# Kernel tuning notes

Hardware: AMD Instinct MI355X
Metric: run time of the kernel (lower is better)

The kernel has to match this reference:

```python
import jax, jax.numpy as jnp
import numpy as np

K_SIZE = 3
CH_IN = 256
NFILT = 256

def setup_inputs() -> dict:
    key = jax.random.key(0)
    k1, k2 = jax.random.split(key)
    x = jax.random.normal(k1, (32, 56, 56, CH_IN), dtype=jnp.float32)
    stdv = 1.0 / np.sqrt(K_SIZE * K_SIZE * CH_IN)
    w = jax.random.normal(k2, (K_SIZE, K_SIZE, CH_IN, NFILT), dtype=jnp.float32) * stdv
    pruning_mask = jnp.ones((K_SIZE * K_SIZE * CH_IN, NFILT), dtype=jnp.float32)
    return {"x": x, "w": w, "pruning_mask": pruning_mask}

def _magnitude_aware_weight(w):
    # scale = mean |w| over (kh, kw, cin), per output filter; stop-gradient
    scale = jax.lax.stop_gradient(jnp.mean(jnp.abs(w), axis=(0, 1, 2), keepdims=True))
    bw_no_grad = scale * jnp.sign(w)
    clipped = jnp.clip(w, -1.0, 1.0)
    # STE: forward = scale*sign(w), backward = d(clip(w,-1,1))
    return jax.lax.stop_gradient(bw_no_grad) - jax.lax.stop_gradient(clipped) + clipped

def reference(x, w, pruning_mask):
    kernel = _magnitude_aware_weight(w) * pruning_mask.reshape(K_SIZE, K_SIZE, CH_IN, NFILT)
    out = jax.lax.conv_general_dilated(
        x, kernel,
        window_strides=(1, 1),
        padding="SAME",
        dimension_numbers=("NHWC", "HWIO", "NHWC"),
    )
    return out
```

## Files before the change

kernel.cpp:

```cpp
#include <hip/hip_runtime.h>

typedef unsigned short u16;
typedef u16 u16x8 __attribute__((ext_vector_type(8)));
typedef __bf16 bf16x8 __attribute__((ext_vector_type(8)));
typedef float f32x4 __attribute__((ext_vector_type(4)));

#define NPIX 100352
#define KTOT 2304
#define IMG_PAD (58 * 58 * 256)

static __device__ __forceinline__ u16 f2bf(float f) {
  unsigned u = __float_as_uint(f);
  return (u16)((u + 0x7fffu + ((u >> 16) & 1u)) >> 16);
}

static __device__ __forceinline__ void gld_lds16(const u16* g, u16* l) {
  __builtin_amdgcn_global_load_lds(
      (const __attribute__((address_space(1))) void*)g,
      (__attribute__((address_space(3))) void*)l, 16, 0, 0);
}

__global__ void scale_accum_k(const float* __restrict__ w, float* __restrict__ scale) {
  const int t = threadIdx.x;
  const float* p = w + (long)blockIdx.x * 64 * 256 + t;
  float acc = 0.f;
#pragma unroll
  for (int e = 0; e < 64; ++e) acc += fabsf(p[(long)e * 256]);
  atomicAdd(&scale[t], acc);
}

__global__ void pack_w_k(const float* __restrict__ w, const float* __restrict__ mask,
                         const float* __restrict__ ssum, u16* __restrict__ wp) {
  __shared__ u16 t[128][33];
  const int k0 = blockIdx.x * 32;
  const int f0 = blockIdx.y * 128;
  const int tid = threadIdx.x;
#pragma unroll
  for (int i = 0; i < 16; ++i) {
    int idx = tid + i * 256;
    int kk = idx >> 7;
    int ff = idx & 127;
    long g = (long)(k0 + kk) * 256 + f0 + ff;
    float wv = w[g];
    float mv = mask[g];
    float sc = ssum[f0 + ff] * (1.0f / 2304.0f);
    float sg = (wv > 0.f) ? 1.f : ((wv < 0.f) ? -1.f : 0.f);
    t[ff][kk] = f2bf(sc * sg * mv);
  }
  __syncthreads();
#pragma unroll
  for (int i = 0; i < 8; ++i) {
    int idx = tid + i * 256;
    int row = idx >> 4;
    int c = idx & 15;
    unsigned v = (unsigned)t[row][2 * c] | ((unsigned)t[row][2 * c + 1] << 16);
    *(unsigned*)(wp + (long)(f0 + row) * KTOT + k0 + 2 * c) = v;
  }
}

__global__ __launch_bounds__(256) void fill_xpad3_k(const float* __restrict__ x,
                                                    u16* __restrict__ xp) {
  const int img = blockIdx.y;
  const int ph = blockIdx.x;
  u16* rowp = xp + ((img * 58 + ph) * 58) * 256;
  const bool irow = (ph >= 1 && ph <= 56);
  const float* xrow = x + ((long)img * 3136 + (ph - 1) * 56) * 256;
  for (int i = threadIdx.x; i < 58 * 32; i += 256) {
    const int pw = i >> 5;
    const int c8 = (i & 31) * 8;
    u16x8 v = {0, 0, 0, 0, 0, 0, 0, 0};
    if (irow && pw >= 1 && pw <= 56) {
      const float* s = xrow + (pw - 1) * 256 + c8;
      float4 a = *(const float4*)s;
      float4 b = *(const float4*)(s + 4);
      v[0] = f2bf(a.x); v[1] = f2bf(a.y); v[2] = f2bf(a.z); v[3] = f2bf(a.w);
      v[4] = f2bf(b.x); v[5] = f2bf(b.y); v[6] = f2bf(b.z); v[7] = f2bf(b.w);
    }
    *(u16x8*)(rowp + pw * 256 + c8) = v;
  }
}

__global__ __launch_bounds__(256) void conv_gemm5_k(
    const u16* __restrict__ xpad, const u16* __restrict__ wp, float* __restrict__ out) {
  __shared__ u16 As[2][128 * 64];
  __shared__ u16 Bs[2][128 * 64];

  const int tid = threadIdx.x;
  const int lane = tid & 63;
  const int wv = tid >> 6;

  const int orig = blockIdx.x;
  const int swz = (orig & 7) * 196 + (orig >> 3);
  const int m0 = (swz >> 1) * 128;
  const int n0 = (swz & 1) * 128;

  const int lsub = lane >> 3;
  const int lc = (lane & 7) ^ (lsub & 7);
  const u16* aptr[4];
  const u16* bptr[4];
#pragma unroll
  for (int i = 0; i < 4; ++i) {
    const int row = (i * 4 + wv) * 8 + lsub;
    const int m = m0 + row;
    const int img = m / 3136, q = m % 3136;
    aptr[i] = xpad + (long)img * IMG_PAD + ((q / 56 + 1) * 58 + (q % 56) + 1) * 256 + lc * 8;
    bptr[i] = wp + (long)(n0 + row) * KTOT + lc * 8;
  }
  const int ldsb = wv * 512;

  const int lm = lane & 15, kq = lane >> 4;
  const int wm = wv & 1, wn = wv >> 1;
  int aoff[2], boff[2];
#pragma unroll
  for (int ct = 0; ct < 2; ++ct) {
    const int pc = ((ct * 4 + kq) ^ (lm & 7)) * 8;
    aoff[ct] = (wm * 64 + lm) * 64 + pc;
    boff[ct] = (wn * 64 + lm) * 64 + pc;
  }

  f32x4 acc[4][4] = {};

  {
    const int ka = -59 * 256;
#pragma unroll
    for (int i = 0; i < 4; ++i) {
      gld_lds16(aptr[i] + ka, As[0] + i * 2048 + ldsb);
      gld_lds16(bptr[i], Bs[0] + i * 2048 + ldsb);
    }
  }

#pragma unroll
  for (int kt = 0; kt < 36; ++kt) {
    const int cur = kt & 1;
    if (kt < 35) {
      const int kn = kt + 1;
      const int khw = kn >> 2;
      const int d = ((khw / 3 - 1) * 58 + (khw % 3 - 1)) * 256;
      const int ka = d + (kn & 3) * 64;
      const int kb = kn * 64;
#pragma unroll
      for (int i = 0; i < 4; ++i) {
        gld_lds16(aptr[i] + ka, As[cur ^ 1] + i * 2048 + ldsb);
        gld_lds16(bptr[i] + kb, Bs[cur ^ 1] + i * 2048 + ldsb);
      }
      asm volatile("s_waitcnt vmcnt(8)" ::: "memory");
    } else {
      asm volatile("s_waitcnt vmcnt(0)" ::: "memory");
    }
    __builtin_amdgcn_s_barrier();
    asm volatile("" ::: "memory");

#pragma unroll
    for (int ct = 0; ct < 2; ++ct) {
      bf16x8 av[4], bv[4];
#pragma unroll
      for (int mi = 0; mi < 4; ++mi) av[mi] = *(const bf16x8*)(As[cur] + aoff[ct] + mi * 1024);
#pragma unroll
      for (int ni = 0; ni < 4; ++ni) bv[ni] = *(const bf16x8*)(Bs[cur] + boff[ct] + ni * 1024);
#pragma unroll
      for (int mi = 0; mi < 4; ++mi)
#pragma unroll
        for (int ni = 0; ni < 4; ++ni)
          acc[mi][ni] = __builtin_amdgcn_mfma_f32_16x16x32_bf16(av[mi], bv[ni], acc[mi][ni], 0, 0, 0);
    }

    asm volatile("" ::: "memory");
    __builtin_amdgcn_s_barrier();
    asm volatile("" ::: "memory");
  }

  float* op = out + (long)(m0 + wm * 64 + kq * 4) * 256 + n0 + wn * 64 + lm;
#pragma unroll
  for (int mi = 0; mi < 4; ++mi) {
#pragma unroll
    for (int ni = 0; ni < 4; ++ni) {
      float* p = op + (long)mi * 16 * 256 + ni * 16;
      f32x4 v = acc[mi][ni];
      p[0] = v[0];
      p[256] = v[1];
      p[512] = v[2];
      p[768] = v[3];
    }
  }
}

__global__ __launch_bounds__(256) void conv_gemm_fb_k(
    const float* __restrict__ x, const u16* __restrict__ wp, float* __restrict__ out) {
  __shared__ u16 As[128 * 40];
  __shared__ u16 Bs[128 * 40];
  const int tid = threadIdx.x;
  const int m0 = blockIdx.x * 128;
  const int n0 = blockIdx.y * 128;
  const int cc = tid & 3;
  const int r0 = tid >> 2;
  const int gm0 = m0 + r0;
  const int gm1 = gm0 + 64;
  const int pix0 = gm0 % 3136, oh0 = pix0 / 56, ow0 = pix0 % 56;
  const int pix1 = gm1 % 3136, oh1 = pix1 / 56, ow1 = pix1 % 56;
  const int lane = tid & 63;
  const int wv = tid >> 6;
  const int wm = wv & 1, wn = wv >> 1;
  const int lm = lane & 15, kq = lane >> 4;
  const int aoff = (wm * 64 + lm) * 40 + kq * 8;
  const int boff = (wn * 64 + lm) * 40 + kq * 8;
  u16* as0 = As + r0 * 40 + cc * 8;
  u16* as1 = As + (r0 + 64) * 40 + cc * 8;
  u16* bs0 = Bs + r0 * 40 + cc * 8;
  u16* bs1 = Bs + (r0 + 64) * 40 + cc * 8;
  const u16* wr0 = wp + (long)(n0 + r0) * KTOT + cc * 8;
  const u16* wr1 = wr0 + (long)64 * KTOT;
  f32x4 acc[4][4] = {};
  for (int khw = 0; khw < 9; ++khw) {
    const int dh = khw / 3 - 1;
    const int dw = khw % 3 - 1;
    const bool v0 = ((unsigned)(oh0 + dh) < 56u) && ((unsigned)(ow0 + dw) < 56u);
    const bool v1 = ((unsigned)(oh1 + dh) < 56u) && ((unsigned)(ow1 + dw) < 56u);
    const long p0 = ((long)gm0 + dh * 56 + dw) * 256 + cc * 8;
    const long p1 = ((long)gm1 + dh * 56 + dw) * 256 + cc * 8;
    const u16* wk0 = wr0 + khw * 256;
    const u16* wk1 = wr1 + khw * 256;
    for (int ct = 0; ct < 8; ++ct) {
      const int ci0 = ct * 32;
      u16x8 a0 = {0,0,0,0,0,0,0,0}, a1 = {0,0,0,0,0,0,0,0};
      float4 l0 = make_float4(0,0,0,0), h0 = make_float4(0,0,0,0);
      float4 l1 = make_float4(0,0,0,0), h1 = make_float4(0,0,0,0);
      if (v0) { l0 = *(const float4*)(x + p0 + ci0); h0 = *(const float4*)(x + p0 + ci0 + 4); }
      if (v1) { l1 = *(const float4*)(x + p1 + ci0); h1 = *(const float4*)(x + p1 + ci0 + 4); }
      a0[0]=f2bf(l0.x); a0[1]=f2bf(l0.y); a0[2]=f2bf(l0.z); a0[3]=f2bf(l0.w);
      a0[4]=f2bf(h0.x); a0[5]=f2bf(h0.y); a0[6]=f2bf(h0.z); a0[7]=f2bf(h0.w);
      a1[0]=f2bf(l1.x); a1[1]=f2bf(l1.y); a1[2]=f2bf(l1.z); a1[3]=f2bf(l1.w);
      a1[4]=f2bf(h1.x); a1[5]=f2bf(h1.y); a1[6]=f2bf(h1.z); a1[7]=f2bf(h1.w);
      u16x8 b0 = *(const u16x8*)(wk0 + ci0);
      u16x8 b1 = *(const u16x8*)(wk1 + ci0);
      __syncthreads();
      *(u16x8*)as0 = a0; *(u16x8*)as1 = a1;
      *(u16x8*)bs0 = b0; *(u16x8*)bs1 = b1;
      __syncthreads();
      bf16x8 av[4], bv[4];
#pragma unroll
      for (int i = 0; i < 4; ++i) av[i] = *(const bf16x8*)(As + aoff + i * 640);
#pragma unroll
      for (int i = 0; i < 4; ++i) bv[i] = *(const bf16x8*)(Bs + boff + i * 640);
#pragma unroll
      for (int mi = 0; mi < 4; ++mi)
#pragma unroll
        for (int ni = 0; ni < 4; ++ni)
          acc[mi][ni] = __builtin_amdgcn_mfma_f32_16x16x32_bf16(av[mi], bv[ni], acc[mi][ni], 0, 0, 0);
    }
  }
  float* op = out + (long)(m0 + wm * 64 + kq * 4) * 256 + n0 + wn * 64 + lm;
#pragma unroll
  for (int mi = 0; mi < 4; ++mi)
#pragma unroll
    for (int ni = 0; ni < 4; ++ni) {
      float* p = op + (long)mi * 16 * 256 + ni * 16;
      f32x4 v = acc[mi][ni];
      p[0] = v[0]; p[256] = v[1]; p[512] = v[2]; p[768] = v[3];
    }
}

extern "C" void kernel_launch(void* const* d_in, const int* in_sizes, int n_in,
                              void* d_out, int out_size, void* d_ws, size_t ws_size,
                              hipStream_t stream) {
  const float* x = (const float*)d_in[0];
  const float* w = (const float*)d_in[1];
  const float* mask = (const float*)d_in[2];
  float* out = (float*)d_out;

  float* scale = (float*)d_ws;
  u16* wp = (u16*)((char*)d_ws + 1088);
  u16* xpad = (u16*)((char*)d_ws + 1088 + 1179648);
  const size_t xpad_bytes = (size_t)32 * IMG_PAD * 2;
  const size_t need = 1088 + 1179648 + xpad_bytes;

  hipMemsetAsync(d_ws, 0, 1088, stream);
  scale_accum_k<<<36, 256, 0, stream>>>(w, scale);
  pack_w_k<<<dim3(72, 2), 256, 0, stream>>>(w, mask, scale, wp);
  if (ws_size >= need) {
    fill_xpad3_k<<<dim3(58, 32), 256, 0, stream>>>(x, xpad);
    conv_gemm5_k<<<1568, 256, 0, stream>>>(xpad, wp, out);
  } else {
    conv_gemm_fb_k<<<dim3(784, 2), 256, 0, stream>>>(x, wp, out);
  }
}
```

Measured before the change: 345.7 us.

## Use 256x256 tiles with 8 waves and interleaved staged loads in conv GEMM

```diff
diff --git a/kernel.cpp b/kernel.cpp
--- a/kernel.cpp
+++ b/kernel.cpp
@@ -18,6 +18,13 @@
   __builtin_amdgcn_global_load_lds(
       (const __attribute__((address_space(1))) void*)g,
       (__attribute__((address_space(3))) void*)l, 16, 0, 0);
+}
+
+static __device__ __forceinline__ int ka_of(int kt) {
+  const int khw = kt >> 2;
+  const int q = (khw * 11) >> 5;
+  const int r = khw - q * 3;
+  return (q * 58 + r - 59) * 256 + (kt & 3) * 64;
 }
 
 __global__ void scale_accum_k(const float* __restrict__ w, float* __restrict__ scale) {
@@ -80,98 +87,150 @@
   }
 }
 
-__global__ __launch_bounds__(256) void conv_gemm5_k(
+#define STAGE_A8(kt, h, b) do { const int _ka = ka_of(kt); \
+    gld_lds16(aptr[(h)*2]     + _ka, As[b] + ldso[(h)*2]); \
+    gld_lds16(aptr[(h)*2 + 1] + _ka, As[b] + ldso[(h)*2 + 1]); } while (0)
+#define STAGE_B8(kt, h, b) do { const int _kb = (kt) * 64; \
+    gld_lds16(bptr[(h)*2]     + _kb, Bs[b] + ldso[(h)*2]); \
+    gld_lds16(bptr[(h)*2 + 1] + _kb, Bs[b] + ldso[(h)*2 + 1]); } while (0)
+
+__global__ __launch_bounds__(512, 2) void conv_gemm8_k(
     const u16* __restrict__ xpad, const u16* __restrict__ wp, float* __restrict__ out) {
-  __shared__ u16 As[2][128 * 64];
-  __shared__ u16 Bs[2][128 * 64];
+  __shared__ u16 As[2][256 * 64];
+  __shared__ u16 Bs[2][256 * 64];
 
   const int tid = threadIdx.x;
   const int lane = tid & 63;
-  const int wv = tid >> 6;
+  const int wid = tid >> 6;
 
   const int orig = blockIdx.x;
-  const int swz = (orig & 7) * 196 + (orig >> 3);
-  const int m0 = (swz >> 1) * 128;
-  const int n0 = (swz & 1) * 128;
+  const int swz = (orig & 7) * 49 + (orig >> 3);
+  const int m0 = swz * 256;
 
   const int lsub = lane >> 3;
-  const int lc = (lane & 7) ^ (lsub & 7);
+  const int lc = (lane & 7) ^ lsub;
   const u16* aptr[4];
   const u16* bptr[4];
-#pragma unroll
-  for (int i = 0; i < 4; ++i) {
-    const int row = (i * 4 + wv) * 8 + lsub;
+  int ldso[4];
+#pragma unroll
+  for (int q = 0; q < 4; ++q) {
+    const int o = (q >> 1) * 16 + (q & 1) * 8 + wid;
+    const int row = o * 8 + lsub;
     const int m = m0 + row;
-    const int img = m / 3136, q = m % 3136;
-    aptr[i] = xpad + (long)img * IMG_PAD + ((q / 56 + 1) * 58 + (q % 56) + 1) * 256 + lc * 8;
-    bptr[i] = wp + (long)(n0 + row) * KTOT + lc * 8;
-  }
-  const int ldsb = wv * 512;
+    const int img = m / 3136, pix = m % 3136;
+    aptr[q] = xpad + (long)img * IMG_PAD + ((pix / 56 + 1) * 58 + (pix % 56) + 1) * 256 + lc * 8;
+    bptr[q] = wp + (long)row * KTOT + lc * 8;
+    ldso[q] = o * 512;
+  }
 
   const int lm = lane & 15, kq = lane >> 4;
-  const int wm = wv & 1, wn = wv >> 1;
-  int aoff[2], boff[2];
-#pragma unroll
-  for (int ct = 0; ct < 2; ++ct) {
-    const int pc = ((ct * 4 + kq) ^ (lm & 7)) * 8;
-    aoff[ct] = (wm * 64 + lm) * 64 + pc;
-    boff[ct] = (wn * 64 + lm) * 64 + pc;
-  }
-
-  f32x4 acc[4][4] = {};
-
-  {
-    const int ka = -59 * 256;
-#pragma unroll
-    for (int i = 0; i < 4; ++i) {
-      gld_lds16(aptr[i] + ka, As[0] + i * 2048 + ldsb);
-      gld_lds16(bptr[i], Bs[0] + i * 2048 + ldsb);
-    }
-  }
-
-#pragma unroll
-  for (int kt = 0; kt < 36; ++kt) {
-    const int cur = kt & 1;
-    if (kt < 35) {
-      const int kn = kt + 1;
-      const int khw = kn >> 2;
-      const int d = ((khw / 3 - 1) * 58 + (khw % 3 - 1)) * 256;
-      const int ka = d + (kn & 3) * 64;
-      const int kb = kn * 64;
-#pragma unroll
-      for (int i = 0; i < 4; ++i) {
-        gld_lds16(aptr[i] + ka, As[cur ^ 1] + i * 2048 + ldsb);
-        gld_lds16(bptr[i] + kb, Bs[cur ^ 1] + i * 2048 + ldsb);
+  const int wm = wid >> 2, wn = wid & 3;
+  int pcq[2];
+  pcq[0] = (kq ^ (lm & 7)) * 8;
+  pcq[1] = ((4 + kq) ^ (lm & 7)) * 8;
+  const int aB = (wm * 128 + lm) * 64;
+  const int bB = (wn * 64 + lm) * 64;
+
+  f32x4 acc[8][4] = {};
+  bf16x8 bv[4][2];
+
+  STAGE_B8(0, 0, 0); STAGE_B8(0, 1, 0);
+  STAGE_A8(0, 0, 0); STAGE_A8(0, 1, 0);
+  STAGE_B8(1, 0, 1); STAGE_B8(1, 1, 1);
+  asm volatile("s_waitcnt vmcnt(4)" ::: "memory");
+  __builtin_amdgcn_s_barrier();
+  asm volatile("" ::: "memory");
+
+  for (int J = 0; J < 17; ++J) {
+#pragma unroll
+    for (int p = 0; p < 8; ++p) {
+      const int buf = p >> 2;
+      const int pp = p & 3;
+      if (pp == 0) {
+#pragma unroll
+        for (int ni = 0; ni < 4; ++ni)
+#pragma unroll
+          for (int ct = 0; ct < 2; ++ct)
+            bv[ni][ct] = *(const bf16x8*)(Bs[buf] + bB + pcq[ct] + ni * 1024);
       }
-      asm volatile("s_waitcnt vmcnt(8)" ::: "memory");
-    } else {
-      asm volatile("s_waitcnt vmcnt(0)" ::: "memory");
-    }
+      bf16x8 av[2][2];
+#pragma unroll
+      for (int f = 0; f < 2; ++f)
+#pragma unroll
+        for (int ct = 0; ct < 2; ++ct)
+          av[f][ct] = *(const bf16x8*)(As[buf] + aB + pcq[ct] + pp * 2048 + f * 1024);
+
+      if (p == 0)      STAGE_A8(2 * J + 1, 0, 1);
+      else if (p == 1) STAGE_A8(2 * J + 1, 1, 1);
+      else if (p == 2) STAGE_B8(2 * J + 2, 0, 0);
+      else if (p == 3) { STAGE_B8(2 * J + 2, 1, 0);
+                         asm volatile("s_waitcnt vmcnt(4)" ::: "memory"); }
+      else if (p == 4) STAGE_A8(2 * J + 2, 0, 0);
+      else if (p == 5) STAGE_A8(2 * J + 2, 1, 0);
+      else if (p == 6) STAGE_B8(2 * J + 3, 0, 1);
+      else             { STAGE_B8(2 * J + 3, 1, 1);
+                         asm volatile("s_waitcnt vmcnt(4)" ::: "memory"); }
+
+      __builtin_amdgcn_s_barrier();
+      asm volatile("" ::: "memory");
+      __builtin_amdgcn_s_setprio(1);
+#pragma unroll
+      for (int ct = 0; ct < 2; ++ct)
+#pragma unroll
+        for (int f = 0; f < 2; ++f)
+#pragma unroll
+          for (int ni = 0; ni < 4; ++ni)
+            acc[pp * 2 + f][ni] = __builtin_amdgcn_mfma_f32_16x16x32_bf16(
+                av[f][ct], bv[ni][ct], acc[pp * 2 + f][ni], 0, 0, 0);
+      __builtin_amdgcn_s_setprio(0);
+      asm volatile("" ::: "memory");
+      __builtin_amdgcn_s_barrier();
+      asm volatile("" ::: "memory");
+    }
+  }
+
+#pragma unroll
+  for (int p = 0; p < 8; ++p) {
+    const int buf = p >> 2;
+    const int pp = p & 3;
+    if (pp == 0) {
+#pragma unroll
+      for (int ni = 0; ni < 4; ++ni)
+#pragma unroll
+        for (int ct = 0; ct < 2; ++ct)
+          bv[ni][ct] = *(const bf16x8*)(Bs[buf] + bB + pcq[ct] + ni * 1024);
+    }
+    bf16x8 av[2][2];
+#pragma unroll
+    for (int f = 0; f < 2; ++f)
+#pragma unroll
+      for (int ct = 0; ct < 2; ++ct)
+        av[f][ct] = *(const bf16x8*)(As[buf] + aB + pcq[ct] + pp * 2048 + f * 1024);
+
+    if (p == 0)      STAGE_A8(35, 0, 1);
+    else if (p == 1) STAGE_A8(35, 1, 1);
+    else if (p == 3) asm volatile("s_waitcnt vmcnt(0)" ::: "memory");
+
     __builtin_amdgcn_s_barrier();
     asm volatile("" ::: "memory");
-
-#pragma unroll
-    for (int ct = 0; ct < 2; ++ct) {
-      bf16x8 av[4], bv[4];
-#pragma unroll
-      for (int mi = 0; mi < 4; ++mi) av[mi] = *(const bf16x8*)(As[cur] + aoff[ct] + mi * 1024);
-#pragma unroll
-      for (int ni = 0; ni < 4; ++ni) bv[ni] = *(const bf16x8*)(Bs[cur] + boff[ct] + ni * 1024);
-#pragma unroll
-      for (int mi = 0; mi < 4; ++mi)
+    __builtin_amdgcn_s_setprio(1);
+#pragma unroll
+    for (int ct = 0; ct < 2; ++ct)
+#pragma unroll
+      for (int f = 0; f < 2; ++f)
 #pragma unroll
         for (int ni = 0; ni < 4; ++ni)
-          acc[mi][ni] = __builtin_amdgcn_mfma_f32_16x16x32_bf16(av[mi], bv[ni], acc[mi][ni], 0, 0, 0);
-    }
-
+          acc[pp * 2 + f][ni] = __builtin_amdgcn_mfma_f32_16x16x32_bf16(
+              av[f][ct], bv[ni][ct], acc[pp * 2 + f][ni], 0, 0, 0);
+    __builtin_amdgcn_s_setprio(0);
     asm volatile("" ::: "memory");
     __builtin_amdgcn_s_barrier();
     asm volatile("" ::: "memory");
   }
 
-  float* op = out + (long)(m0 + wm * 64 + kq * 4) * 256 + n0 + wn * 64 + lm;
-#pragma unroll
-  for (int mi = 0; mi < 4; ++mi) {
+  float* op = out + (long)(m0 + wm * 128 + kq * 4) * 256 + wn * 64 + lm;
+#pragma unroll
+  for (int mi = 0; mi < 8; ++mi) {
 #pragma unroll
     for (int ni = 0; ni < 4; ++ni) {
       float* p = op + (long)mi * 16 * 256 + ni * 16;
@@ -236,16 +295,16 @@
       *(u16x8*)as0 = a0; *(u16x8*)as1 = a1;
       *(u16x8*)bs0 = b0; *(u16x8*)bs1 = b1;
       __syncthreads();
-      bf16x8 av[4], bv[4];
+      bf16x8 av[4], bvv[4];
 #pragma unroll
       for (int i = 0; i < 4; ++i) av[i] = *(const bf16x8*)(As + aoff + i * 640);
 #pragma unroll
-      for (int i = 0; i < 4; ++i) bv[i] = *(const bf16x8*)(Bs + boff + i * 640);
+      for (int i = 0; i < 4; ++i) bvv[i] = *(const bf16x8*)(Bs + boff + i * 640);
 #pragma unroll
       for (int mi = 0; mi < 4; ++mi)
 #pragma unroll
         for (int ni = 0; ni < 4; ++ni)
-          acc[mi][ni] = __builtin_amdgcn_mfma_f32_16x16x32_bf16(av[mi], bv[ni], acc[mi][ni], 0, 0, 0);
+          acc[mi][ni] = __builtin_amdgcn_mfma_f32_16x16x32_bf16(av[mi], bvv[ni], acc[mi][ni], 0, 0, 0);
     }
   }
   float* op = out + (long)(m0 + wm * 64 + kq * 4) * 256 + n0 + wn * 64 + lm;
@@ -278,7 +337,7 @@
   pack_w_k<<<dim3(72, 2), 256, 0, stream>>>(w, mask, scale, wp);
   if (ws_size >= need) {
     fill_xpad3_k<<<dim3(58, 32), 256, 0, stream>>>(x, xpad);
-    conv_gemm5_k<<<1568, 256, 0, stream>>>(xpad, wp, out);
+    conv_gemm8_k<<<392, 512, 0, stream>>>(xpad, wp, out);
   } else {
     conv_gemm_fb_k<<<dim3(784, 2), 256, 0, stream>>>(x, wp, out);
   }
```

New measurement: 335.0 us. 1.03x faster.
